# Performance work log

Hardware: AMD Instinct MI355X
Metric: run time of the kernel (lower is better)

Reference implementation:

```python
import jax, jax.numpy as jnp
import numpy as np

QN = 127.0  # 2^(8-1)-1, symmetric int8
EPS = 1e-5  # batchnorm eps

def ste_round(v):
    return v + jax.lax.stop_gradient(jnp.round(v) - v)

def quant_act(x):
    # HAWQ-style symmetric per-tensor activation quantization (8-bit)
    s = jnp.maximum(jnp.max(jnp.abs(x)) / QN, 1e-8)
    xq = jnp.clip(ste_round(x / s), -QN - 1.0, QN)
    return xq * s, s

def setup_inputs() -> dict:
    key = jax.random.key(0)
    k1, k2, k3, k4, k5, k6 = jax.random.split(key, 6)
    B, Cin, Cout, H, W = 128, 768, 192, 17, 17
    x = jax.random.normal(k1, (B, Cin, H, W), dtype=jnp.float32)
    conv_w = jax.random.normal(k2, (Cout, Cin, 1, 1), dtype=jnp.float32) * 0.02
    bn_gamma = 1.0 + 0.1 * jax.random.normal(k3, (Cout,), dtype=jnp.float32)
    bn_beta = 0.1 * jax.random.normal(k4, (Cout,), dtype=jnp.float32)
    bn_mean = 0.1 * jax.random.normal(k5, (Cout,), dtype=jnp.float32)
    bn_var = 0.5 + jax.random.uniform(k6, (Cout,), dtype=jnp.float32)
    return {"x": x, "conv_w": conv_w, "bn_gamma": bn_gamma, "bn_beta": bn_beta,
            "bn_mean": bn_mean, "bn_var": bn_var, "cluster": 0}

def reference(x, conv_w, bn_gamma, bn_beta, bn_mean, bn_var, cluster):
    # 1) QuantAct on raw input
    x1, s0 = quant_act(x)
    # 2) QuantAveragePool2d (k=3, s=1, p=1, count_include_pad=True): pool in integer domain
    x_int = ste_round(x1 / s0)
    pooled_sum = jax.lax.reduce_window(x_int, 0.0, jax.lax.add,
                                       (1, 1, 3, 3), (1, 1, 1, 1),
                                       [(0, 0), (0, 0), (1, 1), (1, 1)])
    x2 = (pooled_sum / 9.0) * s0
    # 3) QuantAct after pool
    x3, s1 = quant_act(x2)
    # 4) QuantBnConv2d: fold BN into 1x1 conv, per-channel symmetric weight quant
    std = jnp.sqrt(bn_var + EPS)
    w_fold = conv_w * (bn_gamma / std)[:, None, None, None]          # [O,C,1,1]
    b_fold = bn_beta - bn_gamma * bn_mean / std                      # [O]
    w_sf = jnp.maximum(jnp.max(jnp.abs(w_fold), axis=(1, 2, 3)) / QN, 1e-8)  # [O]
    w_int = jnp.clip(ste_round(w_fold / w_sf[:, None, None, None]), -QN - 1.0, QN)
    xi = x3 / s1                                                     # integer-valued acts
    b_int = ste_round(b_fold / (w_sf * s1))
    out_int = jnp.einsum('bchw,oc->bohw', xi, w_int[:, :, 0, 0]) + b_int[None, :, None, None]
    out = out_int * (w_sf * s1)[None, :, None, None]
    # 5) ReLU + output QuantAct
    out = jax.nn.relu(out)
    outq, s2 = quant_act(out)
    return outq, s2
```

## Files before the change

kernel.cpp:

```cpp
#include <hip/hip_runtime.h>
#include <math.h>

#define B_    128
#define C_    768
#define O_    192
#define HW_   289
#define N_IN  (128*768*289)
#define N_OUT (128*192*289)
#define QN_   127.0f

#define SLAB_E   (32*289)
#define SLAB_SH  9248
#define SLAB_BYT 18496
#define QP_LDS   (32*380)

typedef __attribute__((ext_vector_type(4))) int i32x4;

#define SWZ(b) ((b) ^ ((((b) >> 6) & 3) << 4))


__global__ void k_absmax_x(const float4* __restrict__ x4, int n4, unsigned* cnt) {
    float m = 0.f;
    const int stride = gridDim.x * blockDim.x;
    int i = blockIdx.x * blockDim.x + threadIdx.x;
    for (; i + stride < n4; i += 2 * stride) {
        float4 v = x4[i];
        float4 w = x4[i + stride];
        m = fmaxf(m, fmaxf(fmaxf(fabsf(v.x), fabsf(v.y)),
                           fmaxf(fabsf(v.z), fabsf(v.w))));
        m = fmaxf(m, fmaxf(fmaxf(fabsf(w.x), fabsf(w.y)),
                           fmaxf(fabsf(w.z), fabsf(w.w))));
    }
    if (i < n4) {
        float4 v = x4[i];
        m = fmaxf(m, fmaxf(fmaxf(fabsf(v.x), fabsf(v.y)),
                           fmaxf(fabsf(v.z), fabsf(v.w))));
    }
#pragma unroll
    for (int off = 32; off; off >>= 1) m = fmaxf(m, __shfl_down(m, off));
    __shared__ float sm[4];
    int lane = threadIdx.x & 63, wv = threadIdx.x >> 6;
    if (lane == 0) sm[wv] = m;
    __syncthreads();
    if (threadIdx.x == 0) {
        float bm = fmaxf(fmaxf(sm[0], sm[1]), fmaxf(sm[2], sm[3]));
        atomicMax(cnt + 0, __float_as_uint(bm));
    }
}

__launch_bounds__(512) __global__
void k_quant_pool(const float* __restrict__ x, short* __restrict__ pooled,
                  unsigned* cnt) {
    __shared__ __align__(16) float fq[QP_LDS + 8];
    __shared__ int smax[8];
    const int tid = threadIdx.x;
    const int kt = blockIdx.x;
    const int b = blockIdx.z;
    const float s0 = fmaxf(__uint_as_float(cnt[0]) / QN_, 1e-8f);

    for (int i = tid; i < QP_LDS + 8; i += 512) fq[i] = 0.f;
    __syncthreads();

    const float4* xg4 = (const float4*)(x + ((size_t)b * 768 + kt * 32) * HW_);
    for (int t = tid; t < SLAB_E / 4; t += 512) {
        float4 v = xg4[t];
        float q0 = rintf(v.x / s0);
        float q1 = rintf(v.y / s0);
        float q2 = rintf(v.z / s0);
        float q3 = rintf(v.w / s0);
        int e = 4 * t;
#pragma unroll
        for (int j = 0; j < 4; ++j) {
            float q = (j == 0) ? q0 : (j == 1) ? q1 : (j == 2) ? q2 : q3;
            int ej = e + j;
            int p = (ej * 29027) >> 23;
            int i2 = ej - p * 289;
            int r = (i2 * 3856) >> 16;
            int c = i2 - r * 17;
            fq[p * 380 + (r + 1) * 20 + (c + 1)] = q;
        }
    }
    __syncthreads();

    short* slab = pooled + (size_t)(b * 24 + kt) * SLAB_SH;
    int tmax = 0;
    for (int task = tid; task < 2720; task += 512) {
        int p = task & 31;
        int rt = task >> 5;
        int r = (rt * 3277) >> 14;
        int t5 = rt - r * 5;
        int c0 = t5 * 4;
        const float* base = fq + p * 380 + r * 20 + c0;
        float4 a0 = *(const float4*)(base);
        float4 a1 = *(const float4*)(base + 4);
        float4 b0 = *(const float4*)(base + 20);
        float4 b1 = *(const float4*)(base + 24);
        float4 d0 = *(const float4*)(base + 40);
        float4 d1 = *(const float4*)(base + 44);
        float s0c = a0.x + b0.x + d0.x;
        float s1c = a0.y + b0.y + d0.y;
        float s2c = a0.z + b0.z + d0.z;
        float s3c = a0.w + b0.w + d0.w;
        float s4c = a1.x + b1.x + d1.x;
        float s5c = a1.y + b1.y + d1.y;
        int o0 = (int)(s0c + s1c + s2c);
        int o1 = (int)(s1c + s2c + s3c);
        int o2 = (int)(s2c + s3c + s4c);
        int o3 = (int)(s3c + s4c + s5c);
        int i0 = r * 17 + c0;
        slab[(i0 + 0) * 32 + p] = (short)o0;
        int a = o0 < 0 ? -o0 : o0; tmax = a > tmax ? a : tmax;
        if (c0 + 1 < 17) {
            slab[(i0 + 1) * 32 + p] = (short)o1;
            a = o1 < 0 ? -o1 : o1; tmax = a > tmax ? a : tmax;
            slab[(i0 + 2) * 32 + p] = (short)o2;
            a = o2 < 0 ? -o2 : o2; tmax = a > tmax ? a : tmax;
            slab[(i0 + 3) * 32 + p] = (short)o3;
            a = o3 < 0 ? -o3 : o3; tmax = a > tmax ? a : tmax;
        }
    }

#pragma unroll
    for (int off = 32; off; off >>= 1) {
        int o = __shfl_down(tmax, off);
        tmax = o > tmax ? o : tmax;
    }
    if ((tid & 63) == 0) smax[tid >> 6] = tmax;
    __syncthreads();
    if (tid == 0) {
        int bm = smax[0];
#pragma unroll
        for (int i = 1; i < 8; ++i) bm = smax[i] > bm ? smax[i] : bm;
        atomicMax((int*)(cnt + 1), bm);
    }
}

__global__ void k_weights(const float* __restrict__ conv_w,
                          const float* __restrict__ g,
                          const float* __restrict__ beta,
                          const float* __restrict__ mu,
                          const float* __restrict__ var,
                          const unsigned* __restrict__ cnt,
                          signed char* __restrict__ w_q8,
                          float* __restrict__ b_int, float* __restrict__ scale_o,
                          unsigned char* __restrict__ lut8) {
    if (blockIdx.x == O_) {
        const float s0 = fmaxf(__uint_as_float(cnt[0]) / QN_, 1e-8f);
        const float maxx2 = ((float)((const int*)cnt)[1] / 9.0f) * s0;
        const float s1 = fmaxf(maxx2 / QN_, 1e-8f);
        for (int i = threadIdx.x; i < 2305; i += 256) {
            float p = (float)(i - 1152);
            float t = (p / 9.0f) * s0;
            float v = rintf(t / s1);
            v = fminf(fmaxf(v, -128.f), 127.f);
            lut8[i] = (unsigned char)(signed char)(int)v;
        }
        return;
    }
    const int o = blockIdx.x;
    const float stdv = sqrtf(var[o] + 1e-5f);
    const float r = g[o] / stdv;
    const float* wo = conv_w + o * C_;
    float m = 0.f;
    for (int c = threadIdx.x; c < C_; c += 256) m = fmaxf(m, fabsf(wo[c] * r));
#pragma unroll
    for (int off = 32; off; off >>= 1) m = fmaxf(m, __shfl_down(m, off));
    __shared__ float sm[4];
    __shared__ float swsf;
    int lane = threadIdx.x & 63, wv = threadIdx.x >> 6;
    if (lane == 0) sm[wv] = m;
    __syncthreads();
    if (threadIdx.x == 0) {
        float bm = fmaxf(fmaxf(sm[0], sm[1]), fmaxf(sm[2], sm[3]));
        swsf = fmaxf(bm / QN_, 1e-8f);
    }
    __syncthreads();
    const float wsf = swsf;
    for (int c = threadIdx.x; c < C_; c += 256) {
        float wi = rintf(wo[c] * r / wsf);
        wi = fminf(fmaxf(wi, -128.f), 127.f);
        w_q8[(c >> 6) * 12288 + o * 64 + (c & 63)] = (signed char)(int)wi;
    }
    if (threadIdx.x == 0) {
        float s0 = fmaxf(__uint_as_float(cnt[0]) / QN_, 1e-8f);
        float maxx2 = ((float)((const int*)cnt)[1] / 9.0f) * s0;
        float s1 = fmaxf(maxx2 / QN_, 1e-8f);
        float bf = beta[o] - g[o] * mu[o] / stdv;
        b_int[o] = rintf(bf / (wsf * s1));
        scale_o[o] = wsf * s1;
    }
}

__launch_bounds__(256) __global__
void k_gemm(const short* __restrict__ pooled,
            const signed char* __restrict__ w_q8,
            const unsigned char* __restrict__ lut8,
            const float* __restrict__ b_int, const float* __restrict__ scale_o,
            unsigned* cnt, float* __restrict__ out) {
    __shared__ char sW[2][12288];
    __shared__ char sX[2][5120];
    __shared__ unsigned char s_lut[2305];
    __shared__ float red[4];
    const int tid = threadIdx.x;
    const int b = blockIdx.z;
    const int hw0 = blockIdx.x * 80;
    const int L = tid & 63;
    const int wv = tid >> 6;
    const int wo = wv * 48;
    const char* pooled_b = (const char*)pooled;

    for (int i = tid; i < 2305; i += 256) s_lut[i] = lut8[i];

    const int row0 = tid >> 3, ch0 = tid & 7;
    const int row1 = 32 + (tid >> 3), ch1 = tid & 7;
    const int row2 = 64 + (tid >> 3), ch2 = tid & 7;
    const bool act2 = tid < 128;

    uint4 xr0, xr1, xr2;

    auto stageW = [&](int kt, int buf) {
#pragma unroll
        for (int j = 0; j < 3; ++j) {
            int ldsoff = (wv * 3 + j) * 1024;
            const char* src = (const char*)w_q8 + kt * 12288 + SWZ(ldsoff + L * 16);
            __builtin_amdgcn_global_load_lds(
                (const __attribute__((address_space(1))) unsigned int*)src,
                (__attribute__((address_space(3))) unsigned int*)(&sW[buf][0] + ldsoff),
                16, 0, 0);
        }
    };
    auto ldx = [&](int kt, int row, int ch) -> uint4 {
        uint4 z; z.x = z.y = z.z = z.w = 0u;
        int hw = hw0 + row;
        if (hw >= HW_) return z;
        size_t slab = (size_t)(b * 24 + 2 * kt + (ch >> 2)) * SLAB_BYT;
        return *(const uint4*)(pooled_b + slab + hw * 64 + (ch & 3) * 16);
    };
    auto loadX = [&](int kt) {
        xr0 = ldx(kt, row0, ch0);
        xr1 = ldx(kt, row1, ch1);
        if (act2) xr2 = ldx(kt, row2, ch2);
    };
    auto pack8 = [&](const uint4& v) -> uint2 {
        unsigned c0 = s_lut[1152 + (short)(v.x)];
        unsigned c1 = s_lut[1152 + (short)(v.x >> 16)];
        unsigned c2 = s_lut[1152 + (short)(v.y)];
        unsigned c3 = s_lut[1152 + (short)(v.y >> 16)];
        unsigned c4 = s_lut[1152 + (short)(v.z)];
        unsigned c5 = s_lut[1152 + (short)(v.z >> 16)];
        unsigned c6 = s_lut[1152 + (short)(v.w)];
        unsigned c7 = s_lut[1152 + (short)(v.w >> 16)];
        uint2 r;
        r.x = c0 | (c1 << 8) | (c2 << 16) | (c3 << 24);
        r.y = c4 | (c5 << 8) | (c6 << 16) | (c7 << 24);
        return r;
    };
    auto writeX = [&](int buf) {
        *(uint2*)(&sX[buf][0] + SWZ(row0 * 64 + ch0 * 8)) = pack8(xr0);
        *(uint2*)(&sX[buf][0] + SWZ(row1 * 64 + ch1 * 8)) = pack8(xr1);
        if (act2) *(uint2*)(&sX[buf][0] + SWZ(row2 * 64 + ch2 * 8)) = pack8(xr2);
    };

    i32x4 acc[3][5] = {};

    stageW(0, 0);
    loadX(0);
    __syncthreads();
    writeX(0);
    __syncthreads();

    for (int kt = 0; kt < 12; ++kt) {
        const int cur = kt & 1, nxt = cur ^ 1;
        if (kt < 11) {
            stageW(kt + 1, nxt);
            loadX(kt + 1);
        }
        i32x4 af[3], bfr[5];
#pragma unroll
        for (int m = 0; m < 3; ++m)
            af[m] = *(const i32x4*)(&sW[cur][0] +
                SWZ((wo + m * 16 + (L & 15)) * 64 + (L >> 4) * 16));
#pragma unroll
        for (int n = 0; n < 5; ++n)
            bfr[n] = *(const i32x4*)(&sX[cur][0] +
                SWZ((n * 16 + (L & 15)) * 64 + (L >> 4) * 16));
#pragma unroll
        for (int m = 0; m < 3; ++m)
#pragma unroll
            for (int n = 0; n < 5; ++n)
                acc[m][n] = __builtin_amdgcn_mfma_i32_16x16x64_i8(
                    af[m], bfr[n], acc[m][n], 0, 0, 0);
        if (kt < 11) writeX(nxt);
        __syncthreads();
    }

    float lmax = 0.f;
#pragma unroll
    for (int m = 0; m < 3; ++m) {
        int ob = wo + m * 16 + (L >> 4) * 4;
        float bi0 = b_int[ob + 0], bi1 = b_int[ob + 1];
        float bi2 = b_int[ob + 2], bi3 = b_int[ob + 3];
        float sc0 = scale_o[ob + 0], sc1 = scale_o[ob + 1];
        float sc2 = scale_o[ob + 2], sc3 = scale_o[ob + 3];
#pragma unroll
        for (int n = 0; n < 5; ++n) {
            int hw = hw0 + n * 16 + (L & 15);
            if (hw < HW_) {
                size_t base = ((size_t)b * O_ + ob) * HW_ + hw;
                float v0 = fmaxf(((float)acc[m][n][0] + bi0) * sc0, 0.f);
                float v1 = fmaxf(((float)acc[m][n][1] + bi1) * sc1, 0.f);
                float v2 = fmaxf(((float)acc[m][n][2] + bi2) * sc2, 0.f);
                float v3 = fmaxf(((float)acc[m][n][3] + bi3) * sc3, 0.f);
                out[base + 0 * HW_] = v0;
                out[base + 1 * HW_] = v1;
                out[base + 2 * HW_] = v2;
                out[base + 3 * HW_] = v3;
                lmax = fmaxf(fmaxf(fmaxf(v0, v1), fmaxf(v2, v3)), lmax);
            }
        }
    }
#pragma unroll
    for (int off = 32; off; off >>= 1) lmax = fmaxf(lmax, __shfl_down(lmax, off));
    if (L == 0) red[wv] = lmax;
    __syncthreads();
    if (tid == 0) {
        float bm = fmaxf(fmaxf(red[0], red[1]), fmaxf(red[2], red[3]));
        atomicMax(cnt + 2, __float_as_uint(bm));
    }
}

__global__ void k_quant_out(float* __restrict__ out, const unsigned* __restrict__ cnt) {
    const float s2 = fmaxf(__uint_as_float(cnt[2]) / QN_, 1e-8f);
    float4* o4 = (float4*)out;
    const int n4 = N_OUT / 4;
    for (int i = blockIdx.x * blockDim.x + threadIdx.x; i < n4;
         i += gridDim.x * blockDim.x) {
        float4 v = o4[i];
        v.x = fminf(fmaxf(rintf(v.x / s2), -128.f), 127.f) * s2;
        v.y = fminf(fmaxf(rintf(v.y / s2), -128.f), 127.f) * s2;
        v.z = fminf(fmaxf(rintf(v.z / s2), -128.f), 127.f) * s2;
        v.w = fminf(fmaxf(rintf(v.w / s2), -128.f), 127.f) * s2;
        o4[i] = v;
    }
    if (blockIdx.x == 0 && threadIdx.x == 0) out[N_OUT] = s2;
}

extern "C" void kernel_launch(void* const* d_in, const int* in_sizes, int n_in,
                              void* d_out, int out_size, void* d_ws, size_t ws_size,
                              hipStream_t stream) {
    const float* x      = (const float*)d_in[0];
    const float* conv_w = (const float*)d_in[1];
    const float* g      = (const float*)d_in[2];
    const float* beta   = (const float*)d_in[3];
    const float* mu     = (const float*)d_in[4];
    const float* var    = (const float*)d_in[5];
    float* out = (float*)d_out;

    char* wsb = (char*)d_ws;
    unsigned* cnt          = (unsigned*)wsb;
    float* b_int           = (float*)(wsb + 1024);
    float* scale_o         = (float*)(wsb + 2048);
    unsigned char* lut8    = (unsigned char*)(wsb + 3072);
    signed char* w_q8      = (signed char*)(wsb + 8192);
    short* pooled          = (short*)(wsb + (1u << 20));

    hipMemsetAsync(cnt, 0, 16, stream);
    k_absmax_x<<<2048, 256, 0, stream>>>((const float4*)x, N_IN / 4, cnt);
    dim3 qgrid(24, 1, B_);
    k_quant_pool<<<qgrid, 512, 0, stream>>>(x, pooled, cnt);
    k_weights<<<O_ + 1, 256, 0, stream>>>(conv_w, g, beta, mu, var, cnt, w_q8,
                                          b_int, scale_o, lut8);
    dim3 ggrid(4, 1, B_);
    k_gemm<<<ggrid, 256, 0, stream>>>(pooled, w_q8, lut8, b_int, scale_o, cnt, out);
    k_quant_out<<<2048, 256, 0, stream>>>(out, cnt);
}
```

Baseline: 132.3 us.

## Hoist weight quantization ahead of absmax and fold scale LUT into GEMM

```diff
diff --git a/kernel.cpp b/kernel.cpp
--- a/kernel.cpp
+++ b/kernel.cpp
@@ -58,8 +58,19 @@
     const int b = blockIdx.z;
     const float s0 = fmaxf(__uint_as_float(cnt[0]) / QN_, 1e-8f);
 
-    for (int i = tid; i < QP_LDS + 8; i += 512) fq[i] = 0.f;
-    __syncthreads();
+    for (int i = tid; i < 32 * 91; i += 512) {
+        int p = i / 91, rem = i - p * 91;
+        int slot;
+        if (rem < 20) slot = rem;
+        else if (rem < 40) slot = 360 + (rem - 20);
+        else {
+            int t = rem - 40;
+            int rr = t / 3, cc = t - rr * 3;
+            slot = (rr + 1) * 20 + (cc == 0 ? 0 : 17 + cc);
+        }
+        fq[p * 380 + slot] = 0.f;
+    }
+    if (tid < 8) fq[QP_LDS + tid] = 0.f;
 
     const float4* xg4 = (const float4*)(x + ((size_t)b * 768 + kt * 32) * HW_);
     for (int t = tid; t < SLAB_E / 4; t += 512) {
@@ -135,28 +146,13 @@
     }
 }
 
-__global__ void k_weights(const float* __restrict__ conv_w,
-                          const float* __restrict__ g,
-                          const float* __restrict__ beta,
-                          const float* __restrict__ mu,
-                          const float* __restrict__ var,
-                          const unsigned* __restrict__ cnt,
-                          signed char* __restrict__ w_q8,
-                          float* __restrict__ b_int, float* __restrict__ scale_o,
-                          unsigned char* __restrict__ lut8) {
-    if (blockIdx.x == O_) {
-        const float s0 = fmaxf(__uint_as_float(cnt[0]) / QN_, 1e-8f);
-        const float maxx2 = ((float)((const int*)cnt)[1] / 9.0f) * s0;
-        const float s1 = fmaxf(maxx2 / QN_, 1e-8f);
-        for (int i = threadIdx.x; i < 2305; i += 256) {
-            float p = (float)(i - 1152);
-            float t = (p / 9.0f) * s0;
-            float v = rintf(t / s1);
-            v = fminf(fmaxf(v, -128.f), 127.f);
-            lut8[i] = (unsigned char)(signed char)(int)v;
-        }
-        return;
-    }
+__global__ void k_weights_pre(const float* __restrict__ conv_w,
+                              const float* __restrict__ g,
+                              const float* __restrict__ beta,
+                              const float* __restrict__ mu,
+                              const float* __restrict__ var,
+                              signed char* __restrict__ w_q8,
+                              float* __restrict__ wsf_g, float* __restrict__ bf_g) {
     const int o = blockIdx.x;
     const float stdv = sqrtf(var[o] + 1e-5f);
     const float r = g[o] / stdv;
@@ -182,24 +178,21 @@
         w_q8[(c >> 6) * 12288 + o * 64 + (c & 63)] = (signed char)(int)wi;
     }
     if (threadIdx.x == 0) {
-        float s0 = fmaxf(__uint_as_float(cnt[0]) / QN_, 1e-8f);
-        float maxx2 = ((float)((const int*)cnt)[1] / 9.0f) * s0;
-        float s1 = fmaxf(maxx2 / QN_, 1e-8f);
-        float bf = beta[o] - g[o] * mu[o] / stdv;
-        b_int[o] = rintf(bf / (wsf * s1));
-        scale_o[o] = wsf * s1;
+        wsf_g[o] = wsf;
+        bf_g[o] = beta[o] - g[o] * mu[o] / stdv;
     }
 }
 
 __launch_bounds__(256) __global__
 void k_gemm(const short* __restrict__ pooled,
             const signed char* __restrict__ w_q8,
-            const unsigned char* __restrict__ lut8,
-            const float* __restrict__ b_int, const float* __restrict__ scale_o,
+            const float* __restrict__ wsf_g, const float* __restrict__ bf_g,
             unsigned* cnt, float* __restrict__ out) {
     __shared__ char sW[2][12288];
     __shared__ char sX[2][5120];
     __shared__ unsigned char s_lut[2305];
+    __shared__ float s_bint[192];
+    __shared__ float s_scale[192];
     __shared__ float red[4];
     const int tid = threadIdx.x;
     const int b = blockIdx.z;
@@ -209,7 +202,23 @@
     const int wo = wv * 48;
     const char* pooled_b = (const char*)pooled;
 
-    for (int i = tid; i < 2305; i += 256) s_lut[i] = lut8[i];
+    {
+        const float s0 = fmaxf(__uint_as_float(cnt[0]) / QN_, 1e-8f);
+        const float maxx2 = ((float)((const int*)cnt)[1] / 9.0f) * s0;
+        const float s1 = fmaxf(maxx2 / QN_, 1e-8f);
+        for (int i = tid; i < 2305; i += 256) {
+            float p = (float)(i - 1152);
+            float t = (p / 9.0f) * s0;
+            float v = rintf(t / s1);
+            v = fminf(fmaxf(v, -128.f), 127.f);
+            s_lut[i] = (unsigned char)(signed char)(int)v;
+        }
+        if (tid < 192) {
+            float wsf = wsf_g[tid];
+            s_bint[tid] = rintf(bf_g[tid] / (wsf * s1));
+            s_scale[tid] = wsf * s1;
+        }
+    }
 
     const int row0 = tid >> 3, ch0 = tid & 7;
     const int row1 = 32 + (tid >> 3), ch1 = tid & 7;
@@ -298,10 +307,10 @@
 #pragma unroll
     for (int m = 0; m < 3; ++m) {
         int ob = wo + m * 16 + (L >> 4) * 4;
-        float bi0 = b_int[ob + 0], bi1 = b_int[ob + 1];
-        float bi2 = b_int[ob + 2], bi3 = b_int[ob + 3];
-        float sc0 = scale_o[ob + 0], sc1 = scale_o[ob + 1];
-        float sc2 = scale_o[ob + 2], sc3 = scale_o[ob + 3];
+        float bi0 = s_bint[ob + 0], bi1 = s_bint[ob + 1];
+        float bi2 = s_bint[ob + 2], bi3 = s_bint[ob + 3];
+        float sc0 = s_scale[ob + 0], sc1 = s_scale[ob + 1];
+        float sc2 = s_scale[ob + 2], sc3 = s_scale[ob + 3];
 #pragma unroll
         for (int n = 0; n < 5; ++n) {
             int hw = hw0 + n * 16 + (L & 15);
@@ -358,19 +367,18 @@
 
     char* wsb = (char*)d_ws;
     unsigned* cnt          = (unsigned*)wsb;
-    float* b_int           = (float*)(wsb + 1024);
-    float* scale_o         = (float*)(wsb + 2048);
-    unsigned char* lut8    = (unsigned char*)(wsb + 3072);
+    float* wsf_g           = (float*)(wsb + 4096);
+    float* bf_g            = (float*)(wsb + 5120);
     signed char* w_q8      = (signed char*)(wsb + 8192);
     short* pooled          = (short*)(wsb + (1u << 20));
 
     hipMemsetAsync(cnt, 0, 16, stream);
+    k_weights_pre<<<O_, 256, 0, stream>>>(conv_w, g, beta, mu, var, w_q8, wsf_g,
+                                          bf_g);
     k_absmax_x<<<2048, 256, 0, stream>>>((const float4*)x, N_IN / 4, cnt);
     dim3 qgrid(24, 1, B_);
     k_quant_pool<<<qgrid, 512, 0, stream>>>(x, pooled, cnt);
-    k_weights<<<O_ + 1, 256, 0, stream>>>(conv_w, g, beta, mu, var, cnt, w_q8,
-                                          b_int, scale_o, lut8);
     dim3 ggrid(4, 1, B_);
-    k_gemm<<<ggrid, 256, 0, stream>>>(pooled, w_q8, lut8, b_int, scale_o, cnt, out);
+    k_gemm<<<ggrid, 256, 0, stream>>>(pooled, w_q8, wsf_g, bf_g, cnt, out);
     k_quant_out<<<2048, 256, 0, stream>>>(out, cnt);
 }
```

Measured after the change: 129.4 us. 2.2% less time.
